# Kernel optimization log

Measured on AMD Instinct MI355X. Metric: run time of the kernel, lower is better.

## Reference

```python
import jax, jax.numpy as jnp
import numpy as np

LEAKY_SLOPE = 0.01  # torch nn.LeakyReLU default


def _conv_block(x, w, b):
    # 3x3 conv, stride 2, padding 1, then LeakyReLU (ConvBlock.forward)
    y = jax.lax.conv_general_dilated(
        x, w, window_strides=(2, 2), padding=((1, 1), (1, 1)),
        dimension_numbers=('NCHW', 'OIHW', 'NCHW'))
    return jax.nn.leaky_relu(y + b[None, :, None, None], LEAKY_SLOPE)


def _max_pool(x):
    # 2x2 max pool, stride 2 (MaxPoolBlock)
    return jax.lax.reduce_window(x, -jnp.inf, jax.lax.max,
                                 (1, 1, 2, 2), (1, 1, 2, 2), 'VALID')


def _cubic_basis(H):
    # 10 polynomial basis maps built from a Vandermonde matrix (static, HxH)
    x = np.arange(1, H + 1, dtype=np.float64) / H
    v = np.vander(x, increasing=False)
    xa, ya = v, v.T
    maps = np.stack([
        xa ** 3,
        xa ** 2 * ya,
        xa ** 2,
        np.ones_like(xa) + xa * ya ** 2,
        xa * ya,
        xa,
        ya ** 3,
        ya ** 2,
        ya,
        np.ones_like(xa),
    ], axis=0)  # (10, H, H)
    return jnp.asarray(maps, dtype=jnp.float32)


def setup_inputs() -> dict:
    key = jax.random.key(0)
    ks = jax.random.split(key, 12)
    B, C, H = 8, 64, 256
    s = 0.05
    return {
        'feat': jax.random.normal(ks[0], (B, C, H, H), jnp.float32),
        'w1': jax.random.normal(ks[1], (C, C, 3, 3), jnp.float32) * s,
        'b1': jax.random.normal(ks[2], (C,), jnp.float32) * s,
        'w2': jax.random.normal(ks[3], (C, C, 3, 3), jnp.float32) * s,
        'b2': jax.random.normal(ks[4], (C,), jnp.float32) * s,
        'w3': jax.random.normal(ks[5], (C, C, 3, 3), jnp.float32) * s,
        'b3': jax.random.normal(ks[6], (C,), jnp.float32) * s,
        'w4': jax.random.normal(ks[7], (C, C, 3, 3), jnp.float32) * s,
        'b4': jax.random.normal(ks[8], (C,), jnp.float32) * s,
        'fc_w': jax.random.normal(ks[9], (C * 10, C), jnp.float32) * s,
        'fc_b': jax.random.normal(ks[10], (C * 10,), jnp.float32) * s,
    }


def reference(feat, w1, b1, w2, b2, w3, b3, w4, b4, fc_w, fc_b):
    B, C, H, W = feat.shape
    x = _conv_block(feat, w1, b1)   # (B,C,H/2,H/2)
    x = _max_pool(x)
    x = _conv_block(x, w2, b2)
    x = _max_pool(x)
    x = _conv_block(x, w3, b3)
    x = _max_pool(x)
    x = _conv_block(x, w4, b4)      # (B,C,2,2)
    x = jnp.mean(x, axis=(2, 3))    # AdaptiveAvgPool2d(1) + flatten -> (B,C)
    # dropout in eval mode = identity
    R = x @ fc_w.T + fc_b           # (B, C*10)
    basis = _cubic_basis(H)         # (10, H, H)
    # weighted basis sum; equivalent to torch's repeat_interleave + mul + sum
    # but without materializing the (B,C,10,H,W) intermediate
    cubic_mask = jnp.einsum('bck,khw->bchw', R.reshape(B, C, 10), basis)
    return feat + cubic_mask
```

## Files before the change

### kernel.cpp

```cpp
#include <hip/hip_runtime.h>
#include <hip/hip_bf16.h>
#include <cstddef>

#define LEAKY 0.01f

typedef short short8 __attribute__((ext_vector_type(8)));
typedef float f32x4 __attribute__((ext_vector_type(4)));

__device__ inline unsigned short bf16b(float f) {
    __hip_bfloat16 h = __float2bfloat16(f);
    return __builtin_bit_cast(unsigned short, h);
}
__device__ inline float b2f(unsigned short u) {
    unsigned v = (unsigned)u << 16;
    return __builtin_bit_cast(float, v);
}

__global__ __launch_bounds__(256) void wpack_all(const float* __restrict__ w1,
                                                 const float* __restrict__ w2,
                                                 const float* __restrict__ w3,
                                                 const float* __restrict__ w4,
                                                 unsigned short* __restrict__ wpkAll) {
    const float* srcs[4] = {w1, w2, w3, w4};
    const float* w = srcs[blockIdx.y];
    unsigned short* wpk = wpkAll + blockIdx.y * 36864;
    int idx = blockIdx.x * 256 + threadIdx.x;
    int j    = idx & 7;
    int lane = (idx >> 3) & 63;
    int rest = idx >> 9;
    int ks   = rest & 1;
    int mt   = (rest >> 1) & 3;
    int tap  = rest >> 3;
    int co = mt * 16 + (lane & 15);
    int ci = ks * 32 + (lane >> 4) * 8 + j;
    wpk[idx] = bf16b(w[(co * 64 + ci) * 9 + tap]);
}

template<int IH, int IW>
__device__ inline void conv_strip(const unsigned short* __restrict__ inT,
                                  const unsigned short* __restrict__ wpk,
                                  int b, int row, int col0, int lane,
                                  f32x4 acc[4][2]) {
    int n = lane & 15, kg = lane >> 4;
#pragma unroll
    for (int dr = 0; dr < 3; ++dr) {
        int r = 2 * row - 1 + dr;
        if (r < 0) continue;
        const unsigned short* rowp = inT + (((size_t)b * IH + r) * IW) * 64 + kg * 8;
#pragma unroll
        for (int dc = 0; dc < 3; ++dc) {
            int tap = dr * 3 + dc;
            short8 Aw[4][2];
#pragma unroll
            for (int mt = 0; mt < 4; ++mt)
#pragma unroll
                for (int ks = 0; ks < 2; ++ks)
                    Aw[mt][ks] = *(const short8*)(wpk +
                        ((((tap * 4 + mt) * 2 + ks) * 64 + lane) << 3));
            short8 Bx[2][2];
#pragma unroll
            for (int nt = 0; nt < 2; ++nt) {
                int c = 2 * (col0 + nt * 16 + n) - 1 + dc;
                bool ok = c >= 0;
                const unsigned short* p = rowp + (long long)c * 64;
#pragma unroll
                for (int ks = 0; ks < 2; ++ks) {
                    short8 z = {0, 0, 0, 0, 0, 0, 0, 0};
                    if (ok) z = *(const short8*)(p + ks * 32);
                    Bx[nt][ks] = z;
                }
            }
#pragma unroll
            for (int ks = 0; ks < 2; ++ks)
#pragma unroll
                for (int nt = 0; nt < 2; ++nt)
#pragma unroll
                    for (int mt = 0; mt < 4; ++mt)
                        acc[mt][nt] = __builtin_amdgcn_mfma_f32_16x16x32_bf16(
                            Aw[mt][ks], Bx[nt][ks], acc[mt][nt], 0, 0, 0);
        }
    }
}

__device__ inline void epi_to_lds(f32x4 acc[4][2], const float* __restrict__ bias,
                                  unsigned short* Ls, int pixbase, int lane) {
    int n = lane & 15, kg = lane >> 4;
    float4 bias4[4];
#pragma unroll
    for (int mt = 0; mt < 4; ++mt)
        bias4[mt] = *(const float4*)(bias + mt * 16 + kg * 4);
#pragma unroll
    for (int nt = 0; nt < 2; ++nt) {
        int pix = pixbase + nt * 16 + n;
#pragma unroll
        for (int mt = 0; mt < 4; ++mt) {
            float v0 = acc[mt][nt][0] + bias4[mt].x; v0 = v0 > 0.f ? v0 : LEAKY * v0;
            float v1 = acc[mt][nt][1] + bias4[mt].y; v1 = v1 > 0.f ? v1 : LEAKY * v1;
            float v2 = acc[mt][nt][2] + bias4[mt].z; v2 = v2 > 0.f ? v2 : LEAKY * v2;
            float v3 = acc[mt][nt][3] + bias4[mt].w; v3 = v3 > 0.f ? v3 : LEAKY * v3;
            unsigned lo = bf16b(v0) | ((unsigned)bf16b(v1) << 16);
            unsigned hi = bf16b(v2) | ((unsigned)bf16b(v3) << 16);
            int g = mt * 2 + (kg >> 1);
            *(uint2*)(Ls + pix * 64 + (((g ^ (pix & 7)) << 3) + (kg & 1) * 4)) =
                make_uint2(lo, hi);
        }
    }
}

__device__ inline short8 lds_granule(const unsigned short* Ls, int pix, int cig) {
    return *(const short8*)(Ls + pix * 64 + ((cig ^ (pix & 7)) << 3));
}

__global__ __launch_bounds__(256, 4) void conv1f(const float* __restrict__ feat,
                                                 const unsigned short* __restrict__ wpk,
                                                 const float* __restrict__ bias,
                                                 unsigned short* __restrict__ poolT) {
    __shared__ unsigned short Trow[130 * 64];
    __shared__ unsigned short Ls[128 * 64];
    int o = blockIdx.x;
    int blk = (o & 7) * 128 + (o >> 3);
    int half = blk & 1, ohp = (blk >> 1) & 63, b = blk >> 7;
    int tid = threadIdx.x, lane = tid & 63, wv = tid >> 6;
    int n = lane & 15, kg = lane >> 4;
    int c0h = half * 64;
    int colw = (wv & 1) * 32;
    int row_wv = 2 * ohp + (wv >> 1);

    f32x4 acc[4][2] = {};

    int ci0 = tid >> 5, colq = tid & 31;
    const float* fb = feat + (size_t)(b * 64) * 65536;

    for (int r = 4 * ohp - 1; r <= 4 * ohp + 3; ++r) {
        if (r < 0) continue;
        __syncthreads();
#pragma unroll
        for (int k = 0; k < 8; ++k) {
            int cci = ci0 + k * 8;
            float4 f = *(const float4*)(fb + (size_t)cci * 65536 +
                                        (size_t)r * 256 + 2 * c0h + colq * 4);
            float fv[4] = {f.x, f.y, f.z, f.w};
#pragma unroll
            for (int j = 0; j < 4; ++j) {
                int slot = colq * 4 + j + 1;
                int pos = (cci >> 3) ^ ((slot >> 2) & 7);
                Trow[slot * 64 + pos * 8 + (cci & 7)] = bf16b(fv[j]);
            }
        }
        if (tid < 64) {
            float v = (c0h == 0) ? 0.f
                : fb[(size_t)tid * 65536 + (size_t)r * 256 + 2 * c0h - 1];
            Trow[(tid >> 3) * 8 + (tid & 7)] = bf16b(v);
        }
        __syncthreads();
        int dr = r - 2 * row_wv + 1;
        if (dr < 0 || dr > 2) continue;
#pragma unroll
        for (int dc = 0; dc < 3; ++dc) {
            int tap = dr * 3 + dc;
            short8 Aw[4][2];
#pragma unroll
            for (int mt = 0; mt < 4; ++mt)
#pragma unroll
                for (int ks = 0; ks < 2; ++ks)
                    Aw[mt][ks] = *(const short8*)(wpk +
                        ((((tap * 4 + mt) * 2 + ks) * 64 + lane) << 3));
            short8 Bx[2][2];
#pragma unroll
            for (int nt = 0; nt < 2; ++nt) {
                int slot = 2 * (colw + nt * 16 + n) + dc;
#pragma unroll
                for (int ks = 0; ks < 2; ++ks) {
                    int g = ks * 4 + kg;
                    int pos = g ^ ((slot >> 2) & 7);
                    Bx[nt][ks] = *(const short8*)(Trow + slot * 64 + pos * 8);
                }
            }
#pragma unroll
            for (int ks = 0; ks < 2; ++ks)
#pragma unroll
                for (int nt = 0; nt < 2; ++nt)
#pragma unroll
                    for (int mt = 0; mt < 4; ++mt)
                        acc[mt][nt] = __builtin_amdgcn_mfma_f32_16x16x32_bf16(
                            Aw[mt][ks], Bx[nt][ks], acc[mt][nt], 0, 0, 0);
        }
    }

    epi_to_lds(acc, bias, Ls, (wv >> 1) * 64 + colw, lane);
    __syncthreads();

    int px = tid >> 3, cig = tid & 7;
    float m[8];
#pragma unroll
    for (int j = 0; j < 8; ++j) m[j] = -1e30f;
#pragma unroll
    for (int r = 0; r < 2; ++r)
#pragma unroll
        for (int cx = 0; cx < 2; ++cx) {
            short8 v = lds_granule(Ls, r * 64 + 2 * px + cx, cig);
#pragma unroll
            for (int j = 0; j < 8; ++j)
                m[j] = fmaxf(m[j], b2f((unsigned short)v[j]));
        }
    short8 rv;
#pragma unroll
    for (int j = 0; j < 8; ++j)
        rv[j] = (short)(__builtin_bit_cast(unsigned, m[j]) >> 16);
    *(short8*)(poolT + (((size_t)(b * 64 + ohp) * 64) + half * 32 + px) * 64 + cig * 8) = rv;
}

__global__ __launch_bounds__(128) void conv2_pool(const unsigned short* __restrict__ inT,
                                                  const unsigned short* __restrict__ wpk,
                                                  const float* __restrict__ bias,
                                                  unsigned short* __restrict__ poolT) {
    __shared__ unsigned short Ls[64 * 64];
    int o = blockIdx.x;
    int blk = (o & 7) * 16 + (o >> 3);
    int q = blk & 15, b = blk >> 4;
    int tid = threadIdx.x, lane = tid & 63, wv = tid >> 6;

    int row = 2 * q + wv;
    f32x4 acc[4][2] = {};
    conv_strip<64, 64>(inT, wpk, b, row, 0, lane, acc);
    epi_to_lds(acc, bias, Ls, wv * 32, lane);
    __syncthreads();

    int px = tid >> 3, cig = tid & 7;
    float m[8];
#pragma unroll
    for (int j = 0; j < 8; ++j) m[j] = -1e30f;
#pragma unroll
    for (int r = 0; r < 2; ++r)
#pragma unroll
        for (int cx = 0; cx < 2; ++cx) {
            short8 v = lds_granule(Ls, r * 32 + 2 * px + cx, cig);
#pragma unroll
            for (int j = 0; j < 8; ++j)
                m[j] = fmaxf(m[j], b2f((unsigned short)v[j]));
        }
    short8 rv;
#pragma unroll
    for (int j = 0; j < 8; ++j)
        rv[j] = (short)(__builtin_bit_cast(unsigned, m[j]) >> 16);
    *(short8*)(poolT + (((size_t)(b * 16 + q) * 16) + px) * 64 + cig * 8) = rv;
}

__global__ __launch_bounds__(256) void conv3_k(const unsigned short* __restrict__ pool2T,
                                               const unsigned short* __restrict__ wpk3,
                                               const float* __restrict__ bias3,
                                               unsigned short* __restrict__ conv3T) {
    int tid = threadIdx.x, lane = tid & 63, wv = tid >> 6;
    int n = lane & 15, kg = lane >> 4;
    int st = blockIdx.x * 4 + wv;
    f32x4 acc[4][2] = {};
    int bv[2], ohv[2], owv[2];
#pragma unroll
    for (int nt = 0; nt < 2; ++nt) {
        int p = st * 32 + nt * 16 + n;
        bv[nt] = p >> 6; ohv[nt] = (p >> 3) & 7; owv[nt] = p & 7;
    }
#pragma unroll
    for (int dr = 0; dr < 3; ++dr)
#pragma unroll
        for (int dc = 0; dc < 3; ++dc) {
            int tap = dr * 3 + dc;
            short8 Aw[4][2];
#pragma unroll
            for (int mt = 0; mt < 4; ++mt)
#pragma unroll
                for (int ks = 0; ks < 2; ++ks)
                    Aw[mt][ks] = *(const short8*)(wpk3 +
                        ((((tap * 4 + mt) * 2 + ks) * 64 + lane) << 3));
            short8 Bx[2][2];
#pragma unroll
            for (int nt = 0; nt < 2; ++nt) {
                int r = 2 * ohv[nt] - 1 + dr;
                int c = 2 * owv[nt] - 1 + dc;
                bool ok = (r >= 0) && (c >= 0);
                long long off = (((long long)bv[nt] * 16 + r) * 16 + c) * 64 + kg * 8;
#pragma unroll
                for (int ks = 0; ks < 2; ++ks) {
                    short8 z = {0, 0, 0, 0, 0, 0, 0, 0};
                    if (ok) z = *(const short8*)(pool2T + off + ks * 32);
                    Bx[nt][ks] = z;
                }
            }
#pragma unroll
            for (int ks = 0; ks < 2; ++ks)
#pragma unroll
                for (int nt = 0; nt < 2; ++nt)
#pragma unroll
                    for (int mt = 0; mt < 4; ++mt)
                        acc[mt][nt] = __builtin_amdgcn_mfma_f32_16x16x32_bf16(
                            Aw[mt][ks], Bx[nt][ks], acc[mt][nt], 0, 0, 0);
        }
    float4 bias4[4];
#pragma unroll
    for (int mt = 0; mt < 4; ++mt)
        bias4[mt] = *(const float4*)(bias3 + mt * 16 + kg * 4);
#pragma unroll
    for (int nt = 0; nt < 2; ++nt) {
        int pix = st * 32 + nt * 16 + n;
#pragma unroll
        for (int mt = 0; mt < 4; ++mt) {
            float v0 = acc[mt][nt][0] + bias4[mt].x; v0 = v0 > 0.f ? v0 : LEAKY * v0;
            float v1 = acc[mt][nt][1] + bias4[mt].y; v1 = v1 > 0.f ? v1 : LEAKY * v1;
            float v2 = acc[mt][nt][2] + bias4[mt].z; v2 = v2 > 0.f ? v2 : LEAKY * v2;
            float v3 = acc[mt][nt][3] + bias4[mt].w; v3 = v3 > 0.f ? v3 : LEAKY * v3;
            unsigned lo = bf16b(v0) | ((unsigned)bf16b(v1) << 16);
            unsigned hi = bf16b(v2) | ((unsigned)bf16b(v3) << 16);
            *(uint2*)(conv3T + pix * 64 + mt * 16 + kg * 4) = make_uint2(lo, hi);
        }
    }
}

__global__ __launch_bounds__(256) void conv4_k(const unsigned short* __restrict__ conv3T,
                                               const unsigned short* __restrict__ wpk4,
                                               const float* __restrict__ bias4p,
                                               const float* __restrict__ fcw,
                                               const float* __restrict__ fcb,
                                               float* __restrict__ R) {
    __shared__ unsigned short P3s[128 * 64];
    __shared__ float O4s[32 * 64];
    __shared__ float xsS[512];
    int tid = threadIdx.x, lane = tid & 63, wv = tid >> 6;
    int n = lane & 15, kg = lane >> 4;

    for (int i = 0; i < 4; ++i) {
        int task = i * 256 + tid;
        int cig = task & 7, idx = task >> 3;
        int bb = idx >> 4, y = (idx >> 2) & 3, x = idx & 3;
        float m[8];
#pragma unroll
        for (int j = 0; j < 8; ++j) m[j] = -1e30f;
#pragma unroll
        for (int r = 0; r < 2; ++r)
#pragma unroll
            for (int cx = 0; cx < 2; ++cx) {
                int sp = bb * 64 + (2 * y + r) * 8 + (2 * x + cx);
                short8 v = *(const short8*)(conv3T + sp * 64 + cig * 8);
#pragma unroll
                for (int j = 0; j < 8; ++j)
                    m[j] = fmaxf(m[j], b2f((unsigned short)v[j]));
            }
        short8 rv;
#pragma unroll
        for (int j = 0; j < 8; ++j)
            rv[j] = (short)(__builtin_bit_cast(unsigned, m[j]) >> 16);
        *(short8*)(P3s + idx * 64 + ((cig ^ (idx & 7)) << 3)) = rv;
    }
    __syncthreads();

    if (wv == 0) {
        f32x4 acc[4][2] = {};
        int bv[2], ohv[2], owv[2];
#pragma unroll
        for (int nt = 0; nt < 2; ++nt) {
            int p = nt * 16 + n;
            bv[nt] = p >> 2; ohv[nt] = (p >> 1) & 1; owv[nt] = p & 1;
        }
#pragma unroll
        for (int dr = 0; dr < 3; ++dr)
#pragma unroll
            for (int dc = 0; dc < 3; ++dc) {
                int tap = dr * 3 + dc;
                short8 Aw[4][2];
#pragma unroll
                for (int mt = 0; mt < 4; ++mt)
#pragma unroll
                    for (int ks = 0; ks < 2; ++ks)
                        Aw[mt][ks] = *(const short8*)(wpk4 +
                            ((((tap * 4 + mt) * 2 + ks) * 64 + lane) << 3));
                short8 Bx[2][2];
#pragma unroll
                for (int nt = 0; nt < 2; ++nt) {
                    int r = 2 * ohv[nt] - 1 + dr;
                    int c = 2 * owv[nt] - 1 + dc;
                    bool ok = (r >= 0) && (c >= 0);
                    int pix = bv[nt] * 16 + r * 4 + c;
#pragma unroll
                    for (int ks = 0; ks < 2; ++ks) {
                        short8 z = {0, 0, 0, 0, 0, 0, 0, 0};
                        if (ok) z = *(const short8*)(P3s + pix * 64 +
                                     (((ks * 4 + kg) ^ (pix & 7)) << 3));
                        Bx[nt][ks] = z;
                    }
                }
#pragma unroll
                for (int ks = 0; ks < 2; ++ks)
#pragma unroll
                    for (int nt = 0; nt < 2; ++nt)
#pragma unroll
                        for (int mt = 0; mt < 4; ++mt)
                            acc[mt][nt] = __builtin_amdgcn_mfma_f32_16x16x32_bf16(
                                Aw[mt][ks], Bx[nt][ks], acc[mt][nt], 0, 0, 0);
            }
        float4 bias4[4];
#pragma unroll
        for (int mt = 0; mt < 4; ++mt)
            bias4[mt] = *(const float4*)(bias4p + mt * 16 + kg * 4);
#pragma unroll
        for (int nt = 0; nt < 2; ++nt) {
            int p = nt * 16 + n;
#pragma unroll
            for (int mt = 0; mt < 4; ++mt) {
                float4 ov;
                float v0 = acc[mt][nt][0] + bias4[mt].x; ov.x = v0 > 0.f ? v0 : LEAKY * v0;
                float v1 = acc[mt][nt][1] + bias4[mt].y; ov.y = v1 > 0.f ? v1 : LEAKY * v1;
                float v2 = acc[mt][nt][2] + bias4[mt].z; ov.z = v2 > 0.f ? v2 : LEAKY * v2;
                float v3 = acc[mt][nt][3] + bias4[mt].w; ov.w = v3 > 0.f ? v3 : LEAKY * v3;
                *(float4*)(O4s + p * 64 + mt * 16 + kg * 4) = ov;
            }
        }
    }
    __syncthreads();

    for (int i = tid; i < 512; i += 256) {
        int bb = i >> 6, c = i & 63;
        xsS[i] = 0.25f * (O4s[(4 * bb + 0) * 64 + c] + O4s[(4 * bb + 1) * 64 + c] +
                          O4s[(4 * bb + 2) * 64 + c] + O4s[(4 * bb + 3) * 64 + c]);
    }
    __syncthreads();

#pragma unroll
    for (int k = 0; k < 20; ++k) {
        int o = k * 256 + tid;
        int bb = o / 640, i = o - bb * 640;
        float s = fcb[i];
        const float* wr = fcw + i * 64;
        const float* xb = xsS + bb * 64;
#pragma unroll 8
        for (int c = 0; c < 64; ++c) s += xb[c] * wr[c];
        R[o] = s;
    }
}

__global__ __launch_bounds__(256) void final_add_ilp(const float* __restrict__ feat,
                                                     const float* __restrict__ R,
                                                     float* __restrict__ out) {
    int bid = blockIdx.x;
    int q  = bid & 15;
    int bc = bid >> 4;
    int c = bc & 63, b = bc >> 6;
    int tid = threadIdx.x;
    int wq = tid & 63, rg = tid >> 6;
    int w0 = wq * 4;

    const float* Rp = R + (b * 640 + c * 10);
    float r0 = Rp[0], r1 = Rp[1], r2 = Rp[2], r3 = Rp[3], r4 = Rp[4];
    float r5 = Rp[5], r6 = Rp[6], r7 = Rp[7], r8 = Rp[8], r9 = Rp[9];

    float Lw[4], ej[4];
#pragma unroll
    for (int j = 0; j < 4; ++j) {
        Lw[j] = __builtin_amdgcn_logf((float)(w0 + j + 1) * (1.0f / 256.0f));
        ej[j] = (float)(255 - (w0 + j));
    }

    size_t base = ((size_t)(b * 64 + c)) * 65536;
    int h[4];
    float4 f[4];
#pragma unroll
    for (int k = 0; k < 4; ++k) {
        h[k] = q * 16 + k * 4 + rg;
        f[k] = *(const float4*)(feat + base + (size_t)h[k] * 256 + w0);
    }
#pragma unroll
    for (int k = 0; k < 4; ++k) {
        float Lh = __builtin_amdgcn_logf((float)(h[k] + 1) * (1.0f / 256.0f));
        float eh = (float)(255 - h[k]);
        float fv[4] = {f[k].x, f[k].y, f[k].z, f[k].w};
        float ov[4];
#pragma unroll
        for (int j = 0; j < 4; ++j) {
            float a  = __builtin_amdgcn_exp2f(ej[j] * Lh);
            float bb = __builtin_amdgcn_exp2f(eh * Lw[j]);
            float mask = (r9 + r3)
                       + bb * (r8 + bb * (r7 + bb * r6))
                       + a * ((r5 + bb * (r4 + bb * r3))
                              + a * (r2 + bb * r1 + a * r0));
            ov[j] = fv[j] + mask;
        }
        *(float4*)(out + base + (size_t)h[k] * 256 + w0) =
            make_float4(ov[0], ov[1], ov[2], ov[3]);
    }
}

extern "C" void kernel_launch(void* const* d_in, const int* in_sizes, int n_in,
                              void* d_out, int out_size, void* d_ws, size_t ws_size,
                              hipStream_t stream) {
    const float* feat = (const float*)d_in[0];
    const float* w1   = (const float*)d_in[1];
    const float* b1   = (const float*)d_in[2];
    const float* w2   = (const float*)d_in[3];
    const float* b2   = (const float*)d_in[4];
    const float* w3   = (const float*)d_in[5];
    const float* b3   = (const float*)d_in[6];
    const float* w4   = (const float*)d_in[7];
    const float* b4   = (const float*)d_in[8];
    const float* fcw  = (const float*)d_in[9];
    const float* fcb  = (const float*)d_in[10];
    float* out = (float*)d_out;

    unsigned short* wsu    = (unsigned short*)d_ws;
    unsigned short* wpkAll = wsu;
    unsigned short* pool1T = wpkAll + 147456;
    unsigned short* pool2T = pool1T + 2097152;
    unsigned short* conv3T = pool2T + 131072;
    float*          Rm     = (float*)(conv3T + 32768);

    wpack_all<<<dim3(144, 4), 256, 0, stream>>>(w1, w2, w3, w4, wpkAll);
    conv1f<<<1024, 256, 0, stream>>>(feat, wpkAll, b1, pool1T);
    conv2_pool<<<128, 128, 0, stream>>>(pool1T, wpkAll + 36864, b2, pool2T);
    conv3_k<<<4, 256, 0, stream>>>(pool2T, wpkAll + 2 * 36864, b3, conv3T);
    conv4_k<<<1, 256, 0, stream>>>(conv3T, wpkAll + 3 * 36864, b4, fcw, fcb, Rm);
    final_add_ilp<<<8192, 256, 0, stream>>>(feat, Rm, out);
}
```

Before: 142.9 us.

## Double-buffer conv1 input rows and prefetch the next row into registers

The first conv kernel now keeps two LDS row buffers and loads the next input row from global memory into registers while the MFMAs run on the current one, so each step needs one barrier instead of two. The LDS transpose stores are also widened: each thread handles a pair of adjacent channels and writes two packed bf16 values per 32-bit store instead of single 16-bit stores. The Ls buffer for the epilogue now aliases the first row buffer, which needs an extra barrier before the epilogue. The prefetch raises register pressure, which could hurt occupancy at launch_bounds(256,4).

```diff
diff --git a/kernel.cpp b/kernel.cpp
--- a/kernel.cpp
+++ b/kernel.cpp
@@ -115,8 +115,8 @@
                                                  const unsigned short* __restrict__ wpk,
                                                  const float* __restrict__ bias,
                                                  unsigned short* __restrict__ poolT) {
-    __shared__ unsigned short Trow[130 * 64];
-    __shared__ unsigned short Ls[128 * 64];
+    __shared__ unsigned short buf[2][130 * 64];
+    unsigned short* Ls = buf[0];
     int o = blockIdx.x;
     int blk = (o & 7) * 128 + (o >> 3);
     int half = blk & 1, ohp = (blk >> 1) & 63, b = blk >> 7;
@@ -126,67 +126,96 @@
     int colw = (wv & 1) * 32;
     int row_wv = 2 * ohp + (wv >> 1);
 
+    int colq = tid & 31, cipq = tid >> 5;
+    const float* fb = feat + (size_t)(b * 64) * 65536;
+
     f32x4 acc[4][2] = {};
-
-    int ci0 = tid >> 5, colq = tid & 31;
-    const float* fb = feat + (size_t)(b * 64) * 65536;
-
-    for (int r = 4 * ohp - 1; r <= 4 * ohp + 3; ++r) {
-        if (r < 0) continue;
-        __syncthreads();
-#pragma unroll
-        for (int k = 0; k < 8; ++k) {
-            int cci = ci0 + k * 8;
-            float4 f = *(const float4*)(fb + (size_t)cci * 65536 +
-                                        (size_t)r * 256 + 2 * c0h + colq * 4);
-            float fv[4] = {f.x, f.y, f.z, f.w};
+    float4 lo_[4], hi_[4];
+    float edge_ = 0.f;
+
+    auto LOAD = [&](int r) {
+#pragma unroll
+        for (int k = 0; k < 4; ++k) {
+            lo_[k] = make_float4(0.f, 0.f, 0.f, 0.f);
+            hi_[k] = make_float4(0.f, 0.f, 0.f, 0.f);
+        }
+        edge_ = 0.f;
+        if (r >= 0) {
+            const float* rp = fb + (size_t)r * 256 + 2 * c0h + colq * 4;
+#pragma unroll
+            for (int k = 0; k < 4; ++k) {
+                int m = cipq + k * 8;
+                lo_[k] = *(const float4*)(rp + (size_t)(2 * m) * 65536);
+                hi_[k] = *(const float4*)(rp + (size_t)(2 * m + 1) * 65536);
+            }
+            if (tid < 64 && c0h != 0)
+                edge_ = fb[(size_t)tid * 65536 + (size_t)r * 256 + 2 * c0h - 1];
+        }
+    };
+    auto WRITE = [&](unsigned short* B) {
+#pragma unroll
+        for (int k = 0; k < 4; ++k) {
+            int m = cipq + k * 8;
+            int g = m >> 2;
+            int cilow = (2 * m) & 7;
+            float fl[4] = {lo_[k].x, lo_[k].y, lo_[k].z, lo_[k].w};
+            float fh[4] = {hi_[k].x, hi_[k].y, hi_[k].z, hi_[k].w};
 #pragma unroll
             for (int j = 0; j < 4; ++j) {
                 int slot = colq * 4 + j + 1;
-                int pos = (cci >> 3) ^ ((slot >> 2) & 7);
-                Trow[slot * 64 + pos * 8 + (cci & 7)] = bf16b(fv[j]);
+                int pos = g ^ ((slot >> 2) & 7);
+                unsigned pkd = bf16b(fl[j]) | ((unsigned)bf16b(fh[j]) << 16);
+                *(unsigned*)(B + slot * 64 + pos * 8 + cilow) = pkd;
             }
         }
         if (tid < 64) {
-            float v = (c0h == 0) ? 0.f
-                : fb[(size_t)tid * 65536 + (size_t)r * 256 + 2 * c0h - 1];
-            Trow[(tid >> 3) * 8 + (tid & 7)] = bf16b(v);
-        }
+            B[(tid >> 3) * 8 + (tid & 7)] = bf16b(edge_);
+        }
+    };
+
+    int r0 = 4 * ohp - 1;
+    LOAD(r0);
+    WRITE(buf[0]);
+    for (int i = 0; i < 5; ++i) {
+        if (i < 4) LOAD(r0 + i + 1);
         __syncthreads();
-        int dr = r - 2 * row_wv + 1;
-        if (dr < 0 || dr > 2) continue;
-#pragma unroll
-        for (int dc = 0; dc < 3; ++dc) {
-            int tap = dr * 3 + dc;
-            short8 Aw[4][2];
-#pragma unroll
-            for (int mt = 0; mt < 4; ++mt)
+        int dr = (r0 + i) - 2 * row_wv + 1;
+        if (dr >= 0 && dr <= 2) {
+            const unsigned short* T = buf[i & 1];
+#pragma unroll
+            for (int dc = 0; dc < 3; ++dc) {
+                int tap = dr * 3 + dc;
+                short8 Aw[4][2];
+#pragma unroll
+                for (int mt = 0; mt < 4; ++mt)
+#pragma unroll
+                    for (int ks = 0; ks < 2; ++ks)
+                        Aw[mt][ks] = *(const short8*)(wpk +
+                            ((((tap * 4 + mt) * 2 + ks) * 64 + lane) << 3));
+                short8 Bx[2][2];
+#pragma unroll
+                for (int nt = 0; nt < 2; ++nt) {
+                    int slot = 2 * (colw + nt * 16 + n) + dc;
+#pragma unroll
+                    for (int ks = 0; ks < 2; ++ks) {
+                        int pos = (ks * 4 + kg) ^ ((slot >> 2) & 7);
+                        Bx[nt][ks] = *(const short8*)(T + slot * 64 + pos * 8);
+                    }
+                }
 #pragma unroll
                 for (int ks = 0; ks < 2; ++ks)
-                    Aw[mt][ks] = *(const short8*)(wpk +
-                        ((((tap * 4 + mt) * 2 + ks) * 64 + lane) << 3));
-            short8 Bx[2][2];
-#pragma unroll
-            for (int nt = 0; nt < 2; ++nt) {
-                int slot = 2 * (colw + nt * 16 + n) + dc;
-#pragma unroll
-                for (int ks = 0; ks < 2; ++ks) {
-                    int g = ks * 4 + kg;
-                    int pos = g ^ ((slot >> 2) & 7);
-                    Bx[nt][ks] = *(const short8*)(Trow + slot * 64 + pos * 8);
-                }
-            }
-#pragma unroll
-            for (int ks = 0; ks < 2; ++ks)
-#pragma unroll
-                for (int nt = 0; nt < 2; ++nt)
-#pragma unroll
-                    for (int mt = 0; mt < 4; ++mt)
-                        acc[mt][nt] = __builtin_amdgcn_mfma_f32_16x16x32_bf16(
-                            Aw[mt][ks], Bx[nt][ks], acc[mt][nt], 0, 0, 0);
-        }
-    }
-
+#pragma unroll
+                    for (int nt = 0; nt < 2; ++nt)
+#pragma unroll
+                        for (int mt = 0; mt < 4; ++mt)
+                            acc[mt][nt] = __builtin_amdgcn_mfma_f32_16x16x32_bf16(
+                                Aw[mt][ks], Bx[nt][ks], acc[mt][nt], 0, 0, 0);
+            }
+        }
+        if (i < 4) WRITE(buf[(i + 1) & 1]);
+    }
+
+    __syncthreads();
     epi_to_lds(acc, bias, Ls, (wv >> 1) * 64 + colw, lane);
     __syncthreads();
 
```

New measurement: 180.7 us. 26.5% more time.
